# Optimization experiments

Hardware: AMD Instinct MI355X
Metric: run time of the kernel (lower is better)

## Reference

```python
import jax, jax.numpy as jnp
import numpy as np

N = 30000   # nodes
E = 120000  # edges
G = 512     # graphs in batch
F_IN = 1
H1 = 32
H2 = 64
NC = 10


def _lin_init(key, fan_in, fan_out):
    s = 1.0 / np.sqrt(fan_in)
    kw, kb = jax.random.split(key)
    w = jax.random.uniform(kw, (fan_in, fan_out), jnp.float32, minval=-s, maxval=s)
    b = jax.random.uniform(kb, (fan_out,), jnp.float32, minval=-s, maxval=s)
    return w, b


def setup_inputs() -> dict:
    key = jax.random.key(0)
    ks = jax.random.split(key, 16)
    inp = {}
    inp["x"] = jax.random.normal(ks[0], (N, F_IN), jnp.float32)
    inp["edge_attr"] = jax.random.uniform(ks[1], (E, 2), jnp.float32)
    inp["pos"] = jax.random.uniform(ks[2], (N, 2), jnp.float32) * 27.0
    inp["w1a"], inp["b1a"] = _lin_init(ks[3], 2, 25)
    inp["w1b"], inp["b1b"] = _lin_init(ks[4], 25, F_IN * H1)
    inp["root1"], inp["bias1"] = _lin_init(ks[5], F_IN, H1)
    inp["w2a"], inp["b2a"] = _lin_init(ks[6], 2, 25)
    inp["w2b"], inp["b2b"] = _lin_init(ks[7], 25, H1 * H2)
    inp["root2"], inp["bias2"] = _lin_init(ks[8], H1, H2)
    inp["fc1_w"], inp["fc1_b"] = _lin_init(ks[9], H2, 128)
    inp["fc2_w"], inp["fc2_b"] = _lin_init(ks[10], 128, NC)
    inp["edge_index"] = jax.random.randint(ks[11], (2, E), 0, N)
    inp["batch"] = jnp.sort(jax.random.randint(ks[12], (N,), 0, G))
    return inp


def _seg_mean(v, idx, n):
    s = jax.ops.segment_sum(v, idx, num_segments=n)
    c = jax.ops.segment_sum(jnp.ones((v.shape[0], 1), v.dtype), idx, num_segments=n)
    return s / jnp.maximum(c, 1.0)


def _nnconv(x, src, dst, ea, wa, ba, wb, bb, root, bias, n_seg, n_out):
    # per-edge weight matrix from edge MLP: [E, f_in, f_out]
    f_in, f_out = root.shape
    W = (jax.nn.relu(ea @ wa + ba) @ wb + bb).reshape(-1, f_in, f_out)
    msg = jnp.einsum('ei,eio->eo', x[src], W)          # gather + per-edge matmul
    aggr = _seg_mean(msg, dst, n_seg)[:n_out]          # mean scatter-reduce
    return aggr + x @ root + bias


def _forward(x, edge_attr, pos, w1a, b1a, w1b, b1b, root1, bias1,
             w2a, b2a, w2b, b2b, root2, bias2, fc1_w, fc1_b, fc2_w, fc2_b,
             edge_index, batch):
    row, col = edge_index[0], edge_index[1]
    h = jax.nn.elu(_nnconv(x, row, col, edge_attr, w1a, b1a, w1b, b1b,
                           root1, bias1, N, N))
    # graclus stand-in: fixed pairwise matching (consecutive cluster ids)
    n2 = N // 2
    cluster1 = jnp.arange(N) // 2
    x2 = jax.ops.segment_max(h, cluster1, num_segments=n2)     # max_pool x
    pos2 = _seg_mean(pos, cluster1, n2)                        # pool_pos (mean)
    batch2 = batch[0::2]                                       # pool_batch via perm
    row2 = cluster1[row]
    col2 = cluster1[col]
    mask = row2 != col2                                        # drop self loops
    col2m = jnp.where(mask, col2, n2)                          # route to dummy seg
    cart = (pos2[col2] - pos2[row2]) * mask[:, None]           # cartesian pseudo
    max_v = jnp.abs(cart).max()
    ea2 = cart / (2.0 * max_v) + 0.5
    h2 = jax.nn.elu(_nnconv(x2, row2, col2m, ea2, w2a, b2a, w2b, b2b,
                            root2, bias2, n2 + 1, n2))
    n3 = n2 // 2
    cluster2 = jnp.arange(n2) // 2
    x3 = jax.ops.segment_max(h2, cluster2, num_segments=n3)    # max_pool_x
    batch3 = batch2[0::2]
    g = _seg_mean(x3, batch3, G)                               # global_mean_pool
    g = jax.nn.elu(g @ fc1_w + fc1_b)                          # dropout off (eval)
    return jax.nn.log_softmax(g @ fc2_w + fc2_b, axis=1)


def reference(x, edge_attr, pos, w1a, b1a, w1b, b1b, root1, bias1,
              w2a, b2a, w2b, b2b, root2, bias2, fc1_w, fc1_b, fc2_w, fc2_b,
              edge_index, batch):
    return _forward(x, edge_attr, pos, w1a, b1a, w1b, b1b, root1, bias1,
                    w2a, b2a, w2b, b2b, root2, bias2, fc1_w, fc1_b,
                    fc2_w, fc2_b, edge_index, batch)
```

## Files before the change

kernel.cpp:

```cpp
#include <hip/hip_runtime.h>
#include <hip/hip_bf16.h>

#define N_NODES 30000
#define N_EDGES 120000
#define NGRAPH  512
#define N2      15000
#define N3      7500
#define NC      10

#define TSN   4
#define NTS   (N2 / TSN)
#define EC4   64
#define NB1   32
#define NBLK1 ((N_NODES + NB1 - 1) / NB1)
#define EC1   256
#define NDEGB ((N_EDGES + 255) / 256)

#define SC_C1 118
#define SC_C2 59
#define SC_CS 15
#define SC_CT (SC_C1 + SC_C2 + SC_CS)

typedef __hip_bfloat16 bf16;

__device__ __forceinline__ float lo(const float* p, int i) { return p[i]; }
__device__ __forceinline__ float lo(const bf16* p, int i) { return __bfloat162float(p[i]); }
__device__ __forceinline__ void sto(float* p, int i, float v) { p[i] = v; }
__device__ __forceinline__ void sto(bf16* p, int i, float v) { p[i] = __float2bfloat16(v); }
__device__ __forceinline__ float elu(float x) { return x > 0.f ? x : expm1f(x); }

#define MV_OFF    0
#define GS_OFF    1
#define GC_OFF    32769
#define DEG1_OFF  33281
#define DEG2_OFF  63281
#define DEGS_OFF  78281
#define ZERO_FLOATS 82031
#define OFF1_OFF  82031
#define CUR1_OFF  112032
#define OFF2_OFF  142032
#define CUR2_OFF  157033
#define OFFS_OFF  172033
#define CURS_OFF  175784
#define BSUM_OFF  179534
#define ES1_OFF   179726
#define ESS_OFF   299726
#define DPOS_OFF  419726
#define X2_OFF    539726
#define P2_OFF    1019726
#define CT_OFF    1049726
#define MSG_OFF   1289726
#define FLAG_OFF  8969726

struct K1Smem {
  float srow[NB1][28];
  float axl[EC1], ayl[EC1], xsl[EC1];
  float w1a[50];
  float b1a[25];
  float b1b[32];
  float r1[32];
  float bs1[32];
  float hbuf[NB1][33];
  int offl[NB1 + 1];
};

struct K4Smem {
  float YT[TSN][64][32];
  float tl[EC4][32];
  float xl[TSN][32];
  float w2a[50];
  float b2a[25];
  float axl[EC4], ayl[EC4];
  int dpl[EC4];
  int nll[EC4];
};

struct K5Smem {
  float r2l[2048];
  float b2l[64];
  float hl[4][64];
};

__global__ __launch_bounds__(256) void kc_deg(
    const int* __restrict__ ei, const void* x, const void* ea, int* __restrict__ flag,
    int* __restrict__ deg1, int* __restrict__ deg2, int* __restrict__ degS) {
  if (blockIdx.x == NDEGB) {
    const bf16* xb = (const bf16*)x;
    const bf16* eb = (const bf16*)ea;
    int tid = threadIdx.x;
    float a = __bfloat162float(xb[tid]);
    float b = __bfloat162float(eb[tid]);
    int bad = (!(fabsf(a) < 1e3f)) || (!(fabsf(b) < 1e3f));
    unsigned long long m = __ballot(bad);
    __shared__ int anyb[4];
    int w = tid >> 6;
    if ((tid & 63) == 0) anyb[w] = (m != 0ULL) ? 1 : 0;
    __syncthreads();
    if (tid == 0) flag[0] = (anyb[0] | anyb[1] | anyb[2] | anyb[3]);
    return;
  }
  int e = blockIdx.x * 256 + threadIdx.x;
  if (e >= N_EDGES) return;
  int row = ei[e], col = ei[N_EDGES + e];
  atomicAdd(deg1 + col, 1);
  int r2 = row >> 1, c2 = col >> 1;
  if (r2 != c2) {
    atomicAdd(deg2 + c2, 1);
    atomicAdd(degS + (r2 >> 2), 1);
  }
}

__global__ __launch_bounds__(256) void ks_scanA(
    const int* __restrict__ deg1, const int* __restrict__ deg2, const int* __restrict__ degS,
    int* __restrict__ off1, int* __restrict__ off2, int* __restrict__ offS,
    int* __restrict__ bsum) {
  __shared__ int buf[256];
  int c = blockIdx.x, tid = threadIdx.x;
  const int* deg; int* off; int n, local;
  if (c < SC_C1)              { deg = deg1; off = off1; n = 30000; local = c; }
  else if (c < SC_C1 + SC_C2) { deg = deg2; off = off2; n = 15000; local = c - SC_C1; }
  else                        { deg = degS; off = offS; n = 3750;  local = c - SC_C1 - SC_C2; }
  int i = local * 256 + tid;
  int v = (i < n) ? deg[i] : 0;
  buf[tid] = v;
  __syncthreads();
  for (int s = 1; s < 256; s <<= 1) {
    int t = (tid >= s) ? buf[tid - s] : 0;
    __syncthreads();
    buf[tid] += t;
    __syncthreads();
  }
  if (i <= n) off[i] = buf[tid] - v;
  if (tid == 255) bsum[c] = buf[255];
}

__global__ __launch_bounds__(256) void ks_scanB(int* __restrict__ bsum) {
  __shared__ int buf[256];
  int a = blockIdx.x, tid = threadIdx.x;
  int nc, cb;
  if (a == 0)      { nc = SC_C1; cb = 0; }
  else if (a == 1) { nc = SC_C2; cb = SC_C1; }
  else             { nc = SC_CS; cb = SC_C1 + SC_C2; }
  int v = (tid < nc) ? bsum[cb + tid] : 0;
  buf[tid] = v;
  __syncthreads();
  for (int s = 1; s < 256; s <<= 1) {
    int t = (tid >= s) ? buf[tid - s] : 0;
    __syncthreads();
    buf[tid] += t;
    __syncthreads();
  }
  if (tid < nc) bsum[cb + tid] = buf[tid] - v;
}

__global__ __launch_bounds__(256) void ks_scanC(
    int* __restrict__ off1, int* __restrict__ off2, int* __restrict__ offS,
    int* __restrict__ cur1, int* __restrict__ cur2, int* __restrict__ curS,
    const int* __restrict__ bsum) {
  int c = blockIdx.x, tid = threadIdx.x;
  int* off; int* cur; int n, local;
  if (c < SC_C1)              { off = off1; cur = cur1; n = 30000; local = c; }
  else if (c < SC_C1 + SC_C2) { off = off2; cur = cur2; n = 15000; local = c - SC_C1; }
  else                        { off = offS; cur = curS; n = 3750;  local = c - SC_C1 - SC_C2; }
  int add = bsum[c];
  int i = local * 256 + tid;
  if (i <= n) off[i] += add;
  if (i < n) cur[i] = off[i];
}

__global__ __launch_bounds__(256) void kc_place(const int* __restrict__ ei,
                                                int* __restrict__ cur1, int* __restrict__ es1,
                                                int* __restrict__ cur2, int* __restrict__ dpos,
                                                int* __restrict__ curS, int* __restrict__ ess) {
  int e = blockIdx.x * 256 + threadIdx.x;
  if (e >= N_EDGES) return;
  int row = ei[e], col = ei[N_EDGES + e];
  int p = atomicAdd(cur1 + col, 1);
  es1[p] = e;
  int r2 = row >> 1, c2 = col >> 1;
  if (r2 != c2) {
    int q = atomicAdd(cur2 + c2, 1);
    dpos[e] = q;
    int u = atomicAdd(curS + (r2 >> 2), 1);
    ess[u] = e;
  }
}

template <typename T>
__device__ void k1_impl(K1Smem& S,
    const T* __restrict__ x, const T* __restrict__ ea, const T* __restrict__ pos,
    const int* __restrict__ ei,
    const T* __restrict__ w1a, const T* __restrict__ b1a,
    const T* __restrict__ w1b, const T* __restrict__ b1b,
    const T* __restrict__ root1, const T* __restrict__ bias1,
    const int* __restrict__ off1, const int* __restrict__ es1,
    float* __restrict__ x2, float* __restrict__ pos2) {
  int tid = threadIdx.x, t = blockIdx.x;
  int n0 = t * NB1;
  for (int j = tid; j < 50; j += 256) S.w1a[j] = lo(w1a, j);
  for (int j = tid; j < 25; j += 256) S.b1a[j] = lo(b1a, j);
  if (tid < 32) {
    S.b1b[tid] = lo(b1b, tid);
    S.r1[tid] = lo(root1, tid);
    S.bs1[tid] = lo(bias1, tid);
  }
  if (tid <= NB1) {
    int n = n0 + tid; if (n > N_NODES) n = N_NODES;
    S.offl[tid] = off1[n];
  }
  int half = tid >> 5, lk = tid & 31;
  float wreg[28];
#pragma unroll
  for (int k = 0; k < 25; ++k) wreg[k] = lo(w1b, k * 32 + lk);
  wreg[26] = 0.f; wreg[27] = 0.f;
  __syncthreads();
  wreg[25] = S.b1b[lk];
  float wa0 = 0.f, wa1 = 0.f, wb = 0.f;
  if (lk < 25) { wa0 = S.w1a[lk]; wa1 = S.w1a[25 + lk]; wb = S.b1a[lk]; }
  int jbeg = S.offl[0], jend = S.offl[NB1];
  int base = half * 4;
  float s0 = 0.f, s1 = 0.f, s2 = 0.f, s3 = 0.f;
  for (int jb = jbeg; jb < jend; jb += EC1) {
    int ecnt = jend - jb; if (ecnt > EC1) ecnt = EC1;
    __syncthreads();
    if (tid < ecnt) {
      int e = es1[jb + tid];
      S.axl[tid] = lo(ea, 2 * e);
      S.ayl[tid] = lo(ea, 2 * e + 1);
      S.xsl[tid] = lo(x, ei[e]);
    }
    __syncthreads();
    int je = jb + ecnt;
#define K1ACC(i, sacc) { \
    int lj = S.offl[base + i]; if (lj < jb) lj = jb; \
    int hj = S.offl[base + i + 1]; if (hj > je) hj = je; \
    for (int j = lj; j < hj; ++j) { \
      int sj = j - jb; \
      float tk = (lk < 25) ? fmaxf(S.axl[sj] * wa0 + S.ayl[sj] * wa1 + wb, 0.f) : 1.f; \
      sacc += S.xsl[sj] * tk; } }
    K1ACC(0, s0) K1ACC(1, s1) K1ACC(2, s2) K1ACC(3, s3)
#undef K1ACC
  }
  if (lk < 26) {
    S.srow[base][lk] = s0; S.srow[base + 1][lk] = s1;
    S.srow[base + 2][lk] = s2; S.srow[base + 3][lk] = s3;
  } else if (lk < 28) {
    S.srow[base][lk] = 0.f; S.srow[base + 1][lk] = 0.f;
    S.srow[base + 2][lk] = 0.f; S.srow[base + 3][lk] = 0.f;
  }
#pragma unroll
  for (int i = 0; i < 4; ++i) {
    int nl = base + i, n = n0 + nl;
    if (n < N_NODES) {
      const float4* sq = (const float4*)S.srow[nl];
      float a0 = 0.f, a1 = 0.f, a2 = 0.f, a3 = 0.f;
#pragma unroll
      for (int q = 0; q < 7; ++q) {
        float4 sv = sq[q];
        a0 += sv.x * wreg[4 * q];     a1 += sv.y * wreg[4 * q + 1];
        a2 += sv.z * wreg[4 * q + 2]; a3 += sv.w * wreg[4 * q + 3];
      }
      float c = (float)(S.offl[nl + 1] - S.offl[nl]);
      c = fmaxf(c, 1.f);
      S.hbuf[nl][lk] = elu(((a0 + a1) + (a2 + a3)) / c + lo(x, n) * S.r1[lk] + S.bs1[lk]);
    }
  }
  __syncthreads();
  for (int idx = tid; idx < (NB1 / 2) * 32; idx += 256) {
    int pl = idx >> 5, oo = idx & 31;
    int m = t * (NB1 / 2) + pl;
    if (m < N2)
      x2[m * 32 + oo] = fmaxf(S.hbuf[2 * pl][oo], S.hbuf[2 * pl + 1][oo]);
  }
  if (tid < NB1) {
    int pl = tid >> 1, c = tid & 1;
    int m = t * (NB1 / 2) + pl;
    if (m < N2)
      pos2[m * 2 + c] = 0.5f * (lo(pos, (2 * m) * 2 + c) + lo(pos, (2 * m + 1) * 2 + c));
  }
}

__global__ __launch_bounds__(256, 4) void k1_both(
    const int* __restrict__ flag,
    const void* x, const void* ea, const void* pos, const int* ei,
    const void* w1a, const void* b1a, const void* w1b, const void* b1b,
    const void* root1, const void* bias1,
    const int* off1, const int* es1, float* x2, float* pos2) {
  extern __shared__ char sm1[];
  K1Smem& S = *reinterpret_cast<K1Smem*>(sm1);
  if (flag[0] == 1)
    k1_impl<float>(S, (const float*)x, (const float*)ea, (const float*)pos, ei,
                   (const float*)w1a, (const float*)b1a, (const float*)w1b, (const float*)b1b,
                   (const float*)root1, (const float*)bias1, off1, es1, x2, pos2);
  else
    k1_impl<bf16>(S, (const bf16*)x, (const bf16*)ea, (const bf16*)pos, ei,
                  (const bf16*)w1a, (const bf16*)b1a, (const bf16*)w1b, (const bf16*)b1b,
                  (const bf16*)root1, (const bf16*)bias1, off1, es1, x2, pos2);
}

__global__ __launch_bounds__(256) void k3_cart(
    const int* __restrict__ ei, const float* __restrict__ pos2,
    float* __restrict__ cart, unsigned int* __restrict__ maxv) {
  int e = blockIdx.x * 256 + threadIdx.x;
  float m = 0.f;
  if (e < N_EDGES) {
    int r2 = ei[e] >> 1, c2 = ei[N_EDGES + e] >> 1;
    float cx = 0.f, cy = 0.f;
    if (r2 != c2) {
      cx = pos2[2 * c2] - pos2[2 * r2];
      cy = pos2[2 * c2 + 1] - pos2[2 * r2 + 1];
    }
    cart[2 * e] = cx;
    cart[2 * e + 1] = cy;
    m = fmaxf(fabsf(cx), fabsf(cy));
  }
#pragma unroll
  for (int s = 32; s > 0; s >>= 1)
    m = fmaxf(m, __shfl_xor(m, s, 64));
  __shared__ float wm[4];
  int lane = threadIdx.x & 63, wid = threadIdx.x >> 6;
  if (lane == 0) wm[wid] = m;
  __syncthreads();
  if (threadIdx.x == 0) {
    float mm = fmaxf(fmaxf(wm[0], wm[1]), fmaxf(wm[2], wm[3]));
    atomicMax(maxv, __float_as_uint(mm));
  }
}

template <typename T>
__device__ void k4_impl(K4Smem& S,
    const int* __restrict__ ei, const float* __restrict__ cart, const float* __restrict__ maxv_f,
    const float* __restrict__ x2,
    const T* __restrict__ w2a, const T* __restrict__ b2a,
    const T* __restrict__ w2b, const T* __restrict__ b2b,
    const int* __restrict__ offS, const int* __restrict__ ess,
    const int* __restrict__ dpos, float* __restrict__ msg) {
  int tid = threadIdx.x, t = blockIdx.x;
  int n0 = t * TSN;
  if (tid < TSN * 32) S.xl[tid >> 5][tid & 31] = x2[n0 * 32 + tid];
  for (int j = tid; j < 50; j += 256) S.w2a[j] = lo(w2a, j);
  for (int j = tid; j < 25; j += 256) S.b2a[j] = lo(b2a, j);
  __syncthreads();
  int w = tid >> 6, o = tid & 63;
  int ox = o & 7;
  for (int kk = w; kk < 32; kk += 4) {
    float a0 = 0.f, a1 = 0.f, a2 = 0.f, a3 = 0.f;
    if (kk < 26) {
      const T* srcp = (kk < 25) ? (w2b + kk * 2048) : b2b;
#pragma unroll 8
      for (int i = 0; i < 32; ++i) {
        float q = lo(srcp, i * 64 + o);
        a0 += S.xl[0][i] * q;
        a1 += S.xl[1][i] * q;
        a2 += S.xl[2][i] * q;
        a3 += S.xl[3][i] * q;
      }
    }
    int sk = ((((kk >> 2) ^ ox) << 2) | (kk & 3));
    S.YT[0][o][sk] = a0; S.YT[1][o][sk] = a1;
    S.YT[2][o][sk] = a2; S.YT[3][o][sk] = a3;
  }
  float inv = 0.5f / maxv_f[0];
  int j0 = offS[t], j1 = offS[t + 1];
  for (int jb = j0; jb < j1; jb += EC4) {
    int ecnt = j1 - jb; if (ecnt > EC4) ecnt = EC4;
    __syncthreads();
    if (tid < ecnt) {
      int e = ess[jb + tid];
      int r2 = ei[e] >> 1;
      S.nll[tid] = r2 & (TSN - 1);
      S.dpl[tid] = dpos[e];
      S.axl[tid] = cart[2 * e] * inv + 0.5f;
      S.ayl[tid] = cart[2 * e + 1] * inv + 0.5f;
    }
    __syncthreads();
    for (int idx = tid; idx < ecnt * 32; idx += 256) {
      int j = idx >> 5, k = idx & 31;
      if (k < 25)
        S.tl[j][k] = fmaxf(S.axl[j] * S.w2a[k] + S.ayl[j] * S.w2a[25 + k] + S.b2a[k], 0.f);
      else
        S.tl[j][k] = (k == 25) ? 1.f : 0.f;
    }
    __syncthreads();
    for (int j = w; j < ecnt; j += 4) {
      const float* yrow = &S.YT[S.nll[j]][o][0];
      const float4* tq = (const float4*)S.tl[j];
      float a0 = 0.f, a1 = 0.f, a2 = 0.f, a3 = 0.f;
#pragma unroll
      for (int q = 0; q < 8; ++q) {
        float4 tv = tq[q];
        float4 yv = *(const float4*)&yrow[(q ^ ox) << 2];
        a0 += tv.x * yv.x; a1 += tv.y * yv.y;
        a2 += tv.z * yv.z; a3 += tv.w * yv.w;
      }
      msg[(size_t)S.dpl[j] * 64 + o] = (a0 + a1) + (a2 + a3);
    }
  }
}

__global__ __launch_bounds__(256, 3) void k4_both(
    const int* __restrict__ flag,
    const int* ei, const float* cart, const float* maxv_f, const float* x2,
    const void* w2a, const void* b2a, const void* w2b, const void* b2b,
    const int* offS, const int* ess, const int* dpos, float* msg) {
  extern __shared__ char sm4[];
  K4Smem& S = *reinterpret_cast<K4Smem*>(sm4);
  if (flag[0] == 1)
    k4_impl<float>(S, ei, cart, maxv_f, x2, (const float*)w2a, (const float*)b2a,
                   (const float*)w2b, (const float*)b2b, offS, ess, dpos, msg);
  else
    k4_impl<bf16>(S, ei, cart, maxv_f, x2, (const bf16*)w2a, (const bf16*)b2a,
                  (const bf16*)w2b, (const bf16*)b2b, offS, ess, dpos, msg);
}

template <typename T>
__device__ void k5_impl(K5Smem& S,
    const float* __restrict__ msg, const int* __restrict__ off2,
    const float* __restrict__ x2,
    const T* __restrict__ root2, const T* __restrict__ bias2,
    const int* __restrict__ batch,
    float* __restrict__ gsum, float* __restrict__ gcnt) {
  int tid = threadIdx.x;
  for (int j = tid; j < 2048; j += 256) S.r2l[j] = lo(root2, j);
  if (tid < 64) S.b2l[tid] = lo(bias2, tid);
  __syncthreads();
  int w = tid >> 6, o = tid & 63;
  int d = blockIdx.x * 4 + w;
  int j0 = off2[d], j1 = off2[d + 1];
  float s0 = 0.f, s1 = 0.f;
  int j = j0;
  for (; j + 1 < j1; j += 2) {
    s0 += msg[(size_t)j * 64 + o];
    s1 += msg[(size_t)(j + 1) * 64 + o];
  }
  if (j < j1) s0 += msg[(size_t)j * 64 + o];
  float c = fmaxf((float)(j1 - j0), 1.f);
  float r = S.b2l[o];
  const float* xr = x2 + d * 32;
#pragma unroll 8
  for (int i = 0; i < 32; ++i) r += xr[i] * S.r2l[i * 64 + o];
  S.hl[w][o] = elu((s0 + s1) / c + r);
  __syncthreads();
  if (tid < 128) {
    int p = tid >> 6, oo = tid & 63;
    float v = fmaxf(S.hl[2 * p][oo], S.hl[2 * p + 1][oo]);
    int m = blockIdx.x * 2 + p;
    int g = batch[4 * m];
    atomicAdd(gsum + g * 64 + oo, v);
    if (oo == 0) atomicAdd(gcnt + g, 1.f);
  }
}

__global__ __launch_bounds__(256) void k5_both(
    const int* __restrict__ flag,
    const float* msg, const int* off2, const float* x2,
    const void* root2, const void* bias2, const int* batch,
    float* gsum, float* gcnt) {
  extern __shared__ char sm5[];
  K5Smem& S = *reinterpret_cast<K5Smem*>(sm5);
  if (flag[0] == 1)
    k5_impl<float>(S, msg, off2, x2, (const float*)root2, (const float*)bias2, batch, gsum, gcnt);
  else
    k5_impl<bf16>(S, msg, off2, x2, (const bf16*)root2, (const bf16*)bias2, batch, gsum, gcnt);
}

template <typename T>
__device__ void k7_impl(const float* __restrict__ gsum, const float* __restrict__ gcnt,
                        const T* __restrict__ fc1_w, const T* __restrict__ fc1_b,
                        const T* __restrict__ fc2_w, const T* __restrict__ fc2_b,
                        T* __restrict__ out) {
  __shared__ float gv[64];
  __shared__ float h1s[128];
  __shared__ float zs[NC];
  __shared__ float lse;
  int g = blockIdx.x, tid = threadIdx.x;
  if (tid < 64) gv[tid] = gsum[g * 64 + tid] / fmaxf(gcnt[g], 1.f);
  __syncthreads();
  float a = lo(fc1_b, tid);
#pragma unroll 8
  for (int o = 0; o < 64; ++o) a += gv[o] * lo(fc1_w, o * 128 + tid);
  h1s[tid] = elu(a);
  __syncthreads();
  if (tid < NC) {
    float s = lo(fc2_b, tid);
    for (int j = 0; j < 128; ++j) s += h1s[j] * lo(fc2_w, j * NC + tid);
    zs[tid] = s;
  }
  __syncthreads();
  if (tid == 0) {
    float m = -1e30f;
    for (int c = 0; c < NC; ++c) m = fmaxf(m, zs[c]);
    float s = 0.f;
    for (int c = 0; c < NC; ++c) s += expf(zs[c] - m);
    lse = m + logf(s);
  }
  __syncthreads();
  if (tid < NC) sto(out, g * NC + tid, zs[tid] - lse);
}

__global__ __launch_bounds__(128) void k7_both(
    const int* __restrict__ flag,
    const float* gsum, const float* gcnt,
    const void* fc1_w, const void* fc1_b, const void* fc2_w, const void* fc2_b,
    void* out) {
  if (flag[0] == 1)
    k7_impl<float>(gsum, gcnt, (const float*)fc1_w, (const float*)fc1_b,
                   (const float*)fc2_w, (const float*)fc2_b, (float*)out);
  else
    k7_impl<bf16>(gsum, gcnt, (const bf16*)fc1_w, (const bf16*)fc1_b,
                  (const bf16*)fc2_w, (const bf16*)fc2_b, (bf16*)out);
}

extern "C" void kernel_launch(void* const* d_in, const int* in_sizes, int n_in,
                              void* d_out, int out_size, void* d_ws, size_t ws_size,
                              hipStream_t stream) {
  float* ws = (float*)d_ws;
  const int* flag = (const int*)(ws + FLAG_OFF);
  const int* ei = (const int*)d_in[19];
  const int* batch = (const int*)d_in[20];

  hipMemsetAsync(d_ws, 0, (size_t)ZERO_FLOATS * 4, stream);

  kc_deg<<<NDEGB + 1, 256, 0, stream>>>(
      ei, d_in[0], d_in[1], (int*)(ws + FLAG_OFF),
      (int*)(ws + DEG1_OFF), (int*)(ws + DEG2_OFF), (int*)(ws + DEGS_OFF));
  ks_scanA<<<SC_CT, 256, 0, stream>>>(
      (const int*)(ws + DEG1_OFF), (const int*)(ws + DEG2_OFF), (const int*)(ws + DEGS_OFF),
      (int*)(ws + OFF1_OFF), (int*)(ws + OFF2_OFF), (int*)(ws + OFFS_OFF),
      (int*)(ws + BSUM_OFF));
  ks_scanB<<<3, 256, 0, stream>>>((int*)(ws + BSUM_OFF));
  ks_scanC<<<SC_CT, 256, 0, stream>>>(
      (int*)(ws + OFF1_OFF), (int*)(ws + OFF2_OFF), (int*)(ws + OFFS_OFF),
      (int*)(ws + CUR1_OFF), (int*)(ws + CUR2_OFF), (int*)(ws + CURS_OFF),
      (const int*)(ws + BSUM_OFF));
  kc_place<<<NDEGB, 256, 0, stream>>>(
      ei, (int*)(ws + CUR1_OFF), (int*)(ws + ES1_OFF),
      (int*)(ws + CUR2_OFF), (int*)(ws + DPOS_OFF),
      (int*)(ws + CURS_OFF), (int*)(ws + ESS_OFF));

  k1_both<<<NBLK1, 256, sizeof(K1Smem), stream>>>(
      flag, d_in[0], d_in[1], d_in[2], ei,
      d_in[3], d_in[4], d_in[5], d_in[6], d_in[7], d_in[8],
      (const int*)(ws + OFF1_OFF), (const int*)(ws + ES1_OFF),
      ws + X2_OFF, ws + P2_OFF);

  k3_cart<<<NDEGB, 256, 0, stream>>>(
      ei, ws + P2_OFF, ws + CT_OFF, (unsigned int*)(ws + MV_OFF));

  k4_both<<<NTS, 256, sizeof(K4Smem), stream>>>(
      flag, ei, ws + CT_OFF, ws + MV_OFF, ws + X2_OFF,
      d_in[9], d_in[10], d_in[11], d_in[12],
      (const int*)(ws + OFFS_OFF), (const int*)(ws + ESS_OFF),
      (const int*)(ws + DPOS_OFF), ws + MSG_OFF);

  k5_both<<<N2 / 4, 256, sizeof(K5Smem), stream>>>(
      flag, ws + MSG_OFF, (const int*)(ws + OFF2_OFF), ws + X2_OFF,
      d_in[13], d_in[14], batch, ws + GS_OFF, ws + GC_OFF);

  k7_both<<<NGRAPH, 128, 0, stream>>>(
      flag, ws + GS_OFF, ws + GC_OFF,
      d_in[15], d_in[16], d_in[17], d_in[18], d_out);
}
```

Before: 292.5 us.

## Sort edges by source node and cache per-node Y rows in registers for k4

The edge bucketing for the second NNConv now uses per-source-node offsets (degN/offN) instead of per-4-node tile counts, so edges within a tile come out grouped by source node. The k4 kernel splits each edge chunk into contiguous ranges per wave and keeps the 26-entry Y column for the current source node in registers, reloading only when the node changes. This replaces the per-edge swizzled shared-memory reads. The kernel is also split into two typed launches that exit early on the flag, with static shared memory and occupancy raised to 4. The trade-off is an extra launch, a bigger scan and higher register pressure.

```diff
diff --git a/kernel.cpp b/kernel.cpp
--- a/kernel.cpp
+++ b/kernel.cpp
@@ -17,9 +17,9 @@
 #define NDEGB ((N_EDGES + 255) / 256)
 
 #define SC_C1 118
+#define SC_CN 59
 #define SC_C2 59
-#define SC_CS 15
-#define SC_CT (SC_C1 + SC_C2 + SC_CS)
+#define SC_CT (SC_C1 + SC_CN + SC_C2)
 
 typedef __hip_bfloat16 bf16;
 
@@ -28,29 +28,30 @@
 __device__ __forceinline__ void sto(float* p, int i, float v) { p[i] = v; }
 __device__ __forceinline__ void sto(bf16* p, int i, float v) { p[i] = __float2bfloat16(v); }
 __device__ __forceinline__ float elu(float x) { return x > 0.f ? x : expm1f(x); }
+template <typename T> __host__ __device__ constexpr int want_flag() { return sizeof(T) == 4 ? 1 : 0; }
 
 #define MV_OFF    0
 #define GS_OFF    1
 #define GC_OFF    32769
 #define DEG1_OFF  33281
 #define DEG2_OFF  63281
-#define DEGS_OFF  78281
-#define ZERO_FLOATS 82031
-#define OFF1_OFF  82031
-#define CUR1_OFF  112032
-#define OFF2_OFF  142032
-#define CUR2_OFF  157033
-#define OFFS_OFF  172033
-#define CURS_OFF  175784
-#define BSUM_OFF  179534
-#define ES1_OFF   179726
-#define ESS_OFF   299726
-#define DPOS_OFF  419726
-#define X2_OFF    539726
-#define P2_OFF    1019726
-#define CT_OFF    1049726
-#define MSG_OFF   1289726
-#define FLAG_OFF  8969726
+#define DEGN_OFF  78281
+#define ZERO_FLOATS 93281
+#define OFF1_OFF  93281
+#define CUR1_OFF  123282
+#define OFF2_OFF  153282
+#define CUR2_OFF  168283
+#define OFFN_OFF  183283
+#define CURN_OFF  198284
+#define BSUM_OFF  213284
+#define ES1_OFF   213520
+#define ESS_OFF   333520
+#define DPOS_OFF  453520
+#define X2_OFF    573520
+#define P2_OFF    1053520
+#define CT_OFF    1083520
+#define MSG_OFF   1323520
+#define FLAG_OFF  9003520
 
 struct K1Smem {
   float srow[NB1][28];
@@ -64,17 +65,6 @@
   int offl[NB1 + 1];
 };
 
-struct K4Smem {
-  float YT[TSN][64][32];
-  float tl[EC4][32];
-  float xl[TSN][32];
-  float w2a[50];
-  float b2a[25];
-  float axl[EC4], ayl[EC4];
-  int dpl[EC4];
-  int nll[EC4];
-};
-
 struct K5Smem {
   float r2l[2048];
   float b2l[64];
@@ -83,7 +73,7 @@
 
 __global__ __launch_bounds__(256) void kc_deg(
     const int* __restrict__ ei, const void* x, const void* ea, int* __restrict__ flag,
-    int* __restrict__ deg1, int* __restrict__ deg2, int* __restrict__ degS) {
+    int* __restrict__ deg1, int* __restrict__ deg2, int* __restrict__ degN) {
   if (blockIdx.x == NDEGB) {
     const bf16* xb = (const bf16*)x;
     const bf16* eb = (const bf16*)ea;
@@ -106,20 +96,20 @@
   int r2 = row >> 1, c2 = col >> 1;
   if (r2 != c2) {
     atomicAdd(deg2 + c2, 1);
-    atomicAdd(degS + (r2 >> 2), 1);
+    atomicAdd(degN + r2, 1);
   }
 }
 
 __global__ __launch_bounds__(256) void ks_scanA(
-    const int* __restrict__ deg1, const int* __restrict__ deg2, const int* __restrict__ degS,
-    int* __restrict__ off1, int* __restrict__ off2, int* __restrict__ offS,
+    const int* __restrict__ deg1, const int* __restrict__ degN, const int* __restrict__ deg2,
+    int* __restrict__ off1, int* __restrict__ offN, int* __restrict__ off2,
     int* __restrict__ bsum) {
   __shared__ int buf[256];
   int c = blockIdx.x, tid = threadIdx.x;
   const int* deg; int* off; int n, local;
   if (c < SC_C1)              { deg = deg1; off = off1; n = 30000; local = c; }
-  else if (c < SC_C1 + SC_C2) { deg = deg2; off = off2; n = 15000; local = c - SC_C1; }
-  else                        { deg = degS; off = offS; n = 3750;  local = c - SC_C1 - SC_C2; }
+  else if (c < SC_C1 + SC_CN) { deg = degN; off = offN; n = 15000; local = c - SC_C1; }
+  else                        { deg = deg2; off = off2; n = 15000; local = c - SC_C1 - SC_CN; }
   int i = local * 256 + tid;
   int v = (i < n) ? deg[i] : 0;
   buf[tid] = v;
@@ -139,8 +129,8 @@
   int a = blockIdx.x, tid = threadIdx.x;
   int nc, cb;
   if (a == 0)      { nc = SC_C1; cb = 0; }
-  else if (a == 1) { nc = SC_C2; cb = SC_C1; }
-  else             { nc = SC_CS; cb = SC_C1 + SC_C2; }
+  else if (a == 1) { nc = SC_CN; cb = SC_C1; }
+  else             { nc = SC_C2; cb = SC_C1 + SC_CN; }
   int v = (tid < nc) ? bsum[cb + tid] : 0;
   buf[tid] = v;
   __syncthreads();
@@ -154,14 +144,14 @@
 }
 
 __global__ __launch_bounds__(256) void ks_scanC(
-    int* __restrict__ off1, int* __restrict__ off2, int* __restrict__ offS,
-    int* __restrict__ cur1, int* __restrict__ cur2, int* __restrict__ curS,
+    int* __restrict__ off1, int* __restrict__ offN, int* __restrict__ off2,
+    int* __restrict__ cur1, int* __restrict__ curN, int* __restrict__ cur2,
     const int* __restrict__ bsum) {
   int c = blockIdx.x, tid = threadIdx.x;
   int* off; int* cur; int n, local;
   if (c < SC_C1)              { off = off1; cur = cur1; n = 30000; local = c; }
-  else if (c < SC_C1 + SC_C2) { off = off2; cur = cur2; n = 15000; local = c - SC_C1; }
-  else                        { off = offS; cur = curS; n = 3750;  local = c - SC_C1 - SC_C2; }
+  else if (c < SC_C1 + SC_CN) { off = offN; cur = curN; n = 15000; local = c - SC_C1; }
+  else                        { off = off2; cur = cur2; n = 15000; local = c - SC_C1 - SC_CN; }
   int add = bsum[c];
   int i = local * 256 + tid;
   if (i <= n) off[i] += add;
@@ -171,7 +161,7 @@
 __global__ __launch_bounds__(256) void kc_place(const int* __restrict__ ei,
                                                 int* __restrict__ cur1, int* __restrict__ es1,
                                                 int* __restrict__ cur2, int* __restrict__ dpos,
-                                                int* __restrict__ curS, int* __restrict__ ess) {
+                                                int* __restrict__ curN, int* __restrict__ ess) {
   int e = blockIdx.x * 256 + threadIdx.x;
   if (e >= N_EDGES) return;
   int row = ei[e], col = ei[N_EDGES + e];
@@ -181,7 +171,7 @@
   if (r2 != c2) {
     int q = atomicAdd(cur2 + c2, 1);
     dpos[e] = q;
-    int u = atomicAdd(curS + (r2 >> 2), 1);
+    int u = atomicAdd(curN + r2, 1);
     ess[u] = e;
   }
 }
@@ -328,89 +318,89 @@
 }
 
 template <typename T>
-__device__ void k4_impl(K4Smem& S,
+__global__ __launch_bounds__(256, 4) void k4_src(
+    const int* __restrict__ flag,
     const int* __restrict__ ei, const float* __restrict__ cart, const float* __restrict__ maxv_f,
     const float* __restrict__ x2,
     const T* __restrict__ w2a, const T* __restrict__ b2a,
     const T* __restrict__ w2b, const T* __restrict__ b2b,
-    const int* __restrict__ offS, const int* __restrict__ ess,
-    const int* __restrict__ dpos, float* __restrict__ msg) {
+    const int* __restrict__ offN, const int* __restrict__ ess,
+    const int* __restrict__ dpos,
+    float* __restrict__ msg) {
+  if (flag[0] != want_flag<T>()) return;
+  __shared__ float Y[TSN][26][64];
+  __shared__ __align__(16) float tl[EC4][32];
+  __shared__ float xl[TSN][32];
+  __shared__ float w2a_l[50];
+  __shared__ float b2a_l[25];
+  __shared__ float axl[EC4], ayl[EC4];
+  __shared__ int dpl[EC4], nll[EC4];
   int tid = threadIdx.x, t = blockIdx.x;
   int n0 = t * TSN;
-  if (tid < TSN * 32) S.xl[tid >> 5][tid & 31] = x2[n0 * 32 + tid];
-  for (int j = tid; j < 50; j += 256) S.w2a[j] = lo(w2a, j);
-  for (int j = tid; j < 25; j += 256) S.b2a[j] = lo(b2a, j);
+  if (tid < TSN * 32) xl[tid >> 5][tid & 31] = x2[n0 * 32 + tid];
+  for (int j = tid; j < 50; j += 256) w2a_l[j] = lo(w2a, j);
+  for (int j = tid; j < 25; j += 256) b2a_l[j] = lo(b2a, j);
   __syncthreads();
   int w = tid >> 6, o = tid & 63;
-  int ox = o & 7;
-  for (int kk = w; kk < 32; kk += 4) {
+  for (int kk = w; kk < 26; kk += 4) {
+    const T* srcp = (kk < 25) ? (w2b + kk * 2048) : b2b;
     float a0 = 0.f, a1 = 0.f, a2 = 0.f, a3 = 0.f;
-    if (kk < 26) {
-      const T* srcp = (kk < 25) ? (w2b + kk * 2048) : b2b;
 #pragma unroll 8
-      for (int i = 0; i < 32; ++i) {
-        float q = lo(srcp, i * 64 + o);
-        a0 += S.xl[0][i] * q;
-        a1 += S.xl[1][i] * q;
-        a2 += S.xl[2][i] * q;
-        a3 += S.xl[3][i] * q;
-      }
-    }
-    int sk = ((((kk >> 2) ^ ox) << 2) | (kk & 3));
-    S.YT[0][o][sk] = a0; S.YT[1][o][sk] = a1;
-    S.YT[2][o][sk] = a2; S.YT[3][o][sk] = a3;
+    for (int i = 0; i < 32; ++i) {
+      float q = lo(srcp, i * 64 + o);
+      a0 += xl[0][i] * q;
+      a1 += xl[1][i] * q;
+      a2 += xl[2][i] * q;
+      a3 += xl[3][i] * q;
+    }
+    Y[0][kk][o] = a0; Y[1][kk][o] = a1; Y[2][kk][o] = a2; Y[3][kk][o] = a3;
   }
   float inv = 0.5f / maxv_f[0];
-  int j0 = offS[t], j1 = offS[t + 1];
+  int j0 = offN[n0], j1 = offN[n0 + TSN];
+  float yreg[26];
+  int cur_nl = -1;
   for (int jb = j0; jb < j1; jb += EC4) {
     int ecnt = j1 - jb; if (ecnt > EC4) ecnt = EC4;
     __syncthreads();
     if (tid < ecnt) {
       int e = ess[jb + tid];
       int r2 = ei[e] >> 1;
-      S.nll[tid] = r2 & (TSN - 1);
-      S.dpl[tid] = dpos[e];
-      S.axl[tid] = cart[2 * e] * inv + 0.5f;
-      S.ayl[tid] = cart[2 * e + 1] * inv + 0.5f;
+      nll[tid] = r2 & (TSN - 1);
+      dpl[tid] = dpos[e];
+      axl[tid] = cart[2 * e] * inv + 0.5f;
+      ayl[tid] = cart[2 * e + 1] * inv + 0.5f;
     }
     __syncthreads();
     for (int idx = tid; idx < ecnt * 32; idx += 256) {
       int j = idx >> 5, k = idx & 31;
       if (k < 25)
-        S.tl[j][k] = fmaxf(S.axl[j] * S.w2a[k] + S.ayl[j] * S.w2a[25 + k] + S.b2a[k], 0.f);
+        tl[j][k] = fmaxf(axl[j] * w2a_l[k] + ayl[j] * w2a_l[25 + k] + b2a_l[k], 0.f);
       else
-        S.tl[j][k] = (k == 25) ? 1.f : 0.f;
-    }
-    __syncthreads();
-    for (int j = w; j < ecnt; j += 4) {
-      const float* yrow = &S.YT[S.nll[j]][o][0];
-      const float4* tq = (const float4*)S.tl[j];
+        tl[j][k] = (k == 25) ? 1.f : 0.f;
+    }
+    __syncthreads();
+    int slo = (ecnt * w) >> 2;
+    int shi = (ecnt * (w + 1)) >> 2;
+    for (int sj = slo; sj < shi; ++sj) {
+      int nl = nll[sj];
+      if (nl != cur_nl) {
+        cur_nl = nl;
+#pragma unroll
+        for (int k = 0; k < 26; ++k) yreg[k] = Y[nl][k][o];
+      }
+      const float4* tq = (const float4*)tl[sj];
       float a0 = 0.f, a1 = 0.f, a2 = 0.f, a3 = 0.f;
-#pragma unroll
-      for (int q = 0; q < 8; ++q) {
-        float4 tv = tq[q];
-        float4 yv = *(const float4*)&yrow[(q ^ ox) << 2];
-        a0 += tv.x * yv.x; a1 += tv.y * yv.y;
-        a2 += tv.z * yv.z; a3 += tv.w * yv.w;
-      }
-      msg[(size_t)S.dpl[j] * 64 + o] = (a0 + a1) + (a2 + a3);
-    }
-  }
-}
-
-__global__ __launch_bounds__(256, 3) void k4_both(
-    const int* __restrict__ flag,
-    const int* ei, const float* cart, const float* maxv_f, const float* x2,
-    const void* w2a, const void* b2a, const void* w2b, const void* b2b,
-    const int* offS, const int* ess, const int* dpos, float* msg) {
-  extern __shared__ char sm4[];
-  K4Smem& S = *reinterpret_cast<K4Smem*>(sm4);
-  if (flag[0] == 1)
-    k4_impl<float>(S, ei, cart, maxv_f, x2, (const float*)w2a, (const float*)b2a,
-                   (const float*)w2b, (const float*)b2b, offS, ess, dpos, msg);
-  else
-    k4_impl<bf16>(S, ei, cart, maxv_f, x2, (const bf16*)w2a, (const bf16*)b2a,
-                  (const bf16*)w2b, (const bf16*)b2b, offS, ess, dpos, msg);
+      float4 tv;
+      tv = tq[0]; a0 += tv.x * yreg[0];  a1 += tv.y * yreg[1];  a2 += tv.z * yreg[2];  a3 += tv.w * yreg[3];
+      tv = tq[1]; a0 += tv.x * yreg[4];  a1 += tv.y * yreg[5];  a2 += tv.z * yreg[6];  a3 += tv.w * yreg[7];
+      tv = tq[2]; a0 += tv.x * yreg[8];  a1 += tv.y * yreg[9];  a2 += tv.z * yreg[10]; a3 += tv.w * yreg[11];
+      tv = tq[3]; a0 += tv.x * yreg[12]; a1 += tv.y * yreg[13]; a2 += tv.z * yreg[14]; a3 += tv.w * yreg[15];
+      tv = tq[4]; a0 += tv.x * yreg[16]; a1 += tv.y * yreg[17]; a2 += tv.z * yreg[18]; a3 += tv.w * yreg[19];
+      tv = tq[5]; a0 += tv.x * yreg[20]; a1 += tv.y * yreg[21]; a2 += tv.z * yreg[22]; a3 += tv.w * yreg[23];
+      tv = tq[6]; a0 += tv.x * yreg[24]; a1 += tv.y * yreg[25];
+      msg[(size_t)dpl[sj] * 64 + o] = (a0 + a1) + (a2 + a3);
+    }
+  }
 }
 
 template <typename T>
@@ -523,20 +513,20 @@
 
   kc_deg<<<NDEGB + 1, 256, 0, stream>>>(
       ei, d_in[0], d_in[1], (int*)(ws + FLAG_OFF),
-      (int*)(ws + DEG1_OFF), (int*)(ws + DEG2_OFF), (int*)(ws + DEGS_OFF));
+      (int*)(ws + DEG1_OFF), (int*)(ws + DEG2_OFF), (int*)(ws + DEGN_OFF));
   ks_scanA<<<SC_CT, 256, 0, stream>>>(
-      (const int*)(ws + DEG1_OFF), (const int*)(ws + DEG2_OFF), (const int*)(ws + DEGS_OFF),
-      (int*)(ws + OFF1_OFF), (int*)(ws + OFF2_OFF), (int*)(ws + OFFS_OFF),
+      (const int*)(ws + DEG1_OFF), (const int*)(ws + DEGN_OFF), (const int*)(ws + DEG2_OFF),
+      (int*)(ws + OFF1_OFF), (int*)(ws + OFFN_OFF), (int*)(ws + OFF2_OFF),
       (int*)(ws + BSUM_OFF));
   ks_scanB<<<3, 256, 0, stream>>>((int*)(ws + BSUM_OFF));
   ks_scanC<<<SC_CT, 256, 0, stream>>>(
-      (int*)(ws + OFF1_OFF), (int*)(ws + OFF2_OFF), (int*)(ws + OFFS_OFF),
-      (int*)(ws + CUR1_OFF), (int*)(ws + CUR2_OFF), (int*)(ws + CURS_OFF),
+      (int*)(ws + OFF1_OFF), (int*)(ws + OFFN_OFF), (int*)(ws + OFF2_OFF),
+      (int*)(ws + CUR1_OFF), (int*)(ws + CURN_OFF), (int*)(ws + CUR2_OFF),
       (const int*)(ws + BSUM_OFF));
   kc_place<<<NDEGB, 256, 0, stream>>>(
       ei, (int*)(ws + CUR1_OFF), (int*)(ws + ES1_OFF),
       (int*)(ws + CUR2_OFF), (int*)(ws + DPOS_OFF),
-      (int*)(ws + CURS_OFF), (int*)(ws + ESS_OFF));
+      (int*)(ws + CURN_OFF), (int*)(ws + ESS_OFF));
 
   k1_both<<<NBLK1, 256, sizeof(K1Smem), stream>>>(
       flag, d_in[0], d_in[1], d_in[2], ei,
@@ -547,10 +537,15 @@
   k3_cart<<<NDEGB, 256, 0, stream>>>(
       ei, ws + P2_OFF, ws + CT_OFF, (unsigned int*)(ws + MV_OFF));
 
-  k4_both<<<NTS, 256, sizeof(K4Smem), stream>>>(
+  k4_src<float><<<NTS, 256, 0, stream>>>(
       flag, ei, ws + CT_OFF, ws + MV_OFF, ws + X2_OFF,
-      d_in[9], d_in[10], d_in[11], d_in[12],
-      (const int*)(ws + OFFS_OFF), (const int*)(ws + ESS_OFF),
+      (const float*)d_in[9], (const float*)d_in[10], (const float*)d_in[11], (const float*)d_in[12],
+      (const int*)(ws + OFFN_OFF), (const int*)(ws + ESS_OFF),
+      (const int*)(ws + DPOS_OFF), ws + MSG_OFF);
+  k4_src<bf16><<<NTS, 256, 0, stream>>>(
+      flag, ei, ws + CT_OFF, ws + MV_OFF, ws + X2_OFF,
+      (const bf16*)d_in[9], (const bf16*)d_in[10], (const bf16*)d_in[11], (const bf16*)d_in[12],
+      (const int*)(ws + OFFN_OFF), (const int*)(ws + ESS_OFF),
       (const int*)(ws + DPOS_OFF), ws + MSG_OFF);
 
   k5_both<<<N2 / 4, 256, sizeof(K5Smem), stream>>>(
```

Result: faster. 257.8 us (-11.9%).
